# Optimization experiments

Measured on AMD Instinct MI355X. Metric: run time of the kernel, lower is better.

Reference implementation:

```python
import jax, jax.numpy as jnp
import numpy as np

N_NODES = 50000
N_EDGES = 800000
D_IN = 128
D_HID = 128
D_OUT = 128
N_GRAPHS = 512


def _linear_params(key, d_in, d_out):
    kw, kb = jax.random.split(key)
    bound = 1.0 / np.sqrt(d_in)
    W = jax.random.uniform(kw, (d_in, d_out), minval=-bound, maxval=bound, dtype=jnp.float32)
    b = jax.random.uniform(kb, (d_out,), minval=-bound, maxval=bound, dtype=jnp.float32)
    return W, b


def setup_inputs() -> dict:
    key = jax.random.key(0)
    ks = jax.random.split(key, 8)
    x = jax.random.normal(ks[0], (N_NODES, D_IN), dtype=jnp.float32)
    edge_index = jax.random.randint(ks[1], (2, N_EDGES), 0, N_NODES, dtype=jnp.int64)
    batch = jnp.sort(jax.random.randint(ks[2], (N_NODES,), 0, N_GRAPHS, dtype=jnp.int64))
    W1a, b1a = _linear_params(ks[3], D_IN, D_HID)
    W1b, b1b = _linear_params(ks[4], D_HID, D_HID)
    W2a, b2a = _linear_params(ks[5], D_HID, D_HID)
    W2b, b2b = _linear_params(ks[6], D_HID, D_OUT)
    Wfc, bfc = _linear_params(ks[7], D_OUT, D_OUT)
    return {"x": x, "edge_index": edge_index, "batch": batch,
            "W1a": W1a, "b1a": b1a, "W1b": W1b, "b1b": b1b,
            "W2a": W2a, "b2a": b2a, "W2b": W2b, "b2b": b2b,
            "Wfc": Wfc, "bfc": bfc}


def _gin_conv(h, src, dst, Wa, ba, Wb, bb):
    # neighbor sum: gather source features, scatter-add to targets (eps=0)
    agg = jax.ops.segment_sum(h[src], dst, num_segments=N_NODES)
    z = h + agg  # (1+eps)*x + sum_neighbors, eps=0
    z = jax.nn.relu(z @ Wa + ba)
    return z @ Wb + bb


def reference(x, edge_index, batch, W1a, b1a, W1b, b1b, W2a, b2a, W2b, b2b, Wfc, bfc):
    src, dst = edge_index[0], edge_index[1]
    h = jax.nn.relu(_gin_conv(x, src, dst, W1a, b1a, W1b, b1b))
    h = jax.nn.relu(_gin_conv(h, src, dst, W2a, b2a, W2b, b2b))
    g = jax.ops.segment_sum(h, batch, num_segments=N_GRAPHS)  # global_add_pool
    return jax.nn.relu(g @ Wfc + bfc)
```

## Files before the change

### kernel.cpp

```cpp
#include <hip/hip_runtime.h>

#define N_NODES 50000
#define N_EDGES 800000
#define N_GRAPHS 512
#define ZN N_NODES
#define BCAP 1536
#define RCAP 64
#define NBKT 782
#define EPB  8192
#define SCB  ((N_EDGES + EPB - 1) / EPB)

typedef __bf16 bf16x8 __attribute__((ext_vector_type(8)));
typedef float f32x4 __attribute__((ext_vector_type(4)));
typedef unsigned short u16;
typedef unsigned int u32;

__device__ __forceinline__ u16 f2bf(float f) {
    union { float f; u32 i; } v; v.f = f;
    u32 r = v.i + 0x7fffu + ((v.i >> 16) & 1u);
    return (u16)(r >> 16);
}
__device__ __forceinline__ float bf2f(u16 u) {
    union { u32 i; float f; } v; v.i = ((u32)u) << 16; return v.f;
}

__global__ __launch_bounds__(1024)
void k_prep(const int* __restrict__ ei, int* __restrict__ cur, u32* __restrict__ bins,
            const float* __restrict__ X, u16* __restrict__ XB, u16* __restrict__ HB,
            const float* __restrict__ W1a, const float* __restrict__ W1b,
            const float* __restrict__ W2a, const float* __restrict__ W2b,
            u16* __restrict__ T1a, u16* __restrict__ T1b,
            u16* __restrict__ T2a, u16* __restrict__ T2b,
            int E, int n8) {
    __shared__ int lcnt[NBKT];
    __shared__ int lpos[NBKT];
    int bid = blockIdx.x;
    int t = threadIdx.x;
    if (bid < SCB) {
        for (int i = t; i < NBKT; i += 1024) lcnt[i] = 0;
        __syncthreads();
        int e0 = bid * EPB;
        int sarr[8], barr[8], dlar[8];
#pragma unroll
        for (int k = 0; k < 8; ++k) {
            int e = e0 + k * 1024 + t;
            if (e < E) {
                int s = ei[e];
                int d = ei[E + e];
                sarr[k] = s; barr[k] = d >> 6; dlar[k] = d & 63;
                atomicAdd(&lcnt[d >> 6], 1);
            } else {
                barr[k] = -1; sarr[k] = 0; dlar[k] = 0;
            }
        }
        __syncthreads();
        for (int i = t; i < NBKT; i += 1024) {
            int c = lcnt[i];
            lpos[i] = (c > 0) ? atomicAdd(&cur[i * 32], c) : 0;
        }
        __syncthreads();
#pragma unroll
        for (int k = 0; k < 8; ++k) {
            if (barr[k] >= 0) {
                int p = atomicAdd(&lpos[barr[k]], 1);
                if (p < BCAP)
                    bins[(size_t)barr[k] * BCAP + p] = (((u32)dlar[k]) << 16) | (u32)sarr[k];
            }
        }
    } else if (bid < SCB + 782) {
        int i = (bid - SCB) * 1024 + t;
        if (i < n8) {
            float4 v0 = ((const float4*)X)[i * 2];
            float4 v1 = ((const float4*)X)[i * 2 + 1];
            uint4 o;
            o.x = (u32)f2bf(v0.x) | (((u32)f2bf(v0.y)) << 16);
            o.y = (u32)f2bf(v0.z) | (((u32)f2bf(v0.w)) << 16);
            o.z = (u32)f2bf(v1.x) | (((u32)f2bf(v1.y)) << 16);
            o.w = (u32)f2bf(v1.z) | (((u32)f2bf(v1.w)) << 16);
            ((uint4*)XB)[i] = o;
        }
    } else if (bid < SCB + 782 + 64) {
        int b2 = bid - (SCB + 782);
        int widx = b2 >> 4;
        int i = (b2 & 15) * 1024 + t;
        const float* W = widx == 0 ? W1a : widx == 1 ? W1b : widx == 2 ? W2a : W2b;
        u16* T = widx == 0 ? T1a : widx == 1 ? T1b : widx == 2 ? T2a : T2b;
        int k = i >> 7, n = i & 127;
        T[n * 128 + k] = f2bf(W[k * 128 + n]);
    } else {
        if (t < 64)       ((u32*)XB)[(size_t)ZN * 64 + t]        = 0u;
        else if (t < 128) ((u32*)HB)[(size_t)ZN * 64 + (t - 64)] = 0u;
    }
}


#define STAGE16(BUF, CI, CJ)                                            \
    _Pragma("unroll")                                                   \
    for (int u = 0; u < 16; ++u) {                                      \
        u32 nb = (u32)smI[wv * 8 + (CI)][(CJ) + u];                     \
        BUF[u] = X2[(nb << 6) + lane];                                  \
    }

#define ACCUM16(BUF)                                                    \
    _Pragma("unroll")                                                   \
    for (int u = 0; u < 16; ++u) {                                      \
        ax += bf2f((u16)(BUF[u] & 0xffff));                             \
        ay += bf2f((u16)(BUF[u] >> 16));                                \
    }

#define FINROW(CI) {                                                    \
        int r = wv * 8 + (CI);                                          \
        smZu[(r * 16 + ((lane >> 2) ^ (r & 15))) * 4 + (lane & 3)] =    \
            (((u32)f2bf(ay)) << 16) | (u32)f2bf(ax);                    \
        ax = 0.f; ay = 0.f;                                             \
    }

#define AGG_PHASE()                                                                  \
    {                                                                                \
        const u32 fill = 0xC350C350u;                      \
        int r = tid >> 3, c = tid & 7;                                               \
        uint4 v4 = make_uint4(fill, fill, fill, fill);                               \
        if (c == 0) {                                                                \
            int gr = row0 + r;                                                       \
            v4.x = (fill & 0xffff0000u) | (u32)((gr < N) ? gr : ZN);                 \
        }                                                                            \
        ((uint4*)smI)[tid] = v4;                                                     \
        if (tid < 64) ldsCnt[tid] = 1;                                               \
    }                                                                                \
    __syncthreads();                                                                 \
    {                                                                                \
        int ecnt = cur[blockIdx.x * 32];                                             \
        if (ecnt > BCAP) ecnt = BCAP;                                                \
        const u32* myb = bins + (size_t)blockIdx.x * BCAP;                           \
        for (int i = tid; i < ecnt; i += 512) {                                      \
            u32 v = myb[i];                                                          \
            int dl = v >> 16;                                                        \
            int pos = atomicAdd(&ldsCnt[dl], 1);                                     \
            if (pos < RCAP) smI[dl][pos] = (u16)(v & 0xffff);                        \
        }                                                                            \
    }                                                                                \
    __syncthreads();                                                                 \
    int degv = 0;                                                                    \
    if (lane < 8) {                                                                  \
        int d = ldsCnt[wv * 8 + lane];                                               \
        degv = d > RCAP ? RCAP : d;                                                  \
    }                                                                                \
    {                                                                                \
        float ax = 0.f, ay = 0.f;                                                    \
        u32 bufA[16], bufB[16];                                                      \
        int ci = 0, cj = 0;                                                          \
        int de = __builtin_amdgcn_readlane(degv, 0);                                 \
        STAGE16(bufA, 0, 0);                                                         \
        for (;;) {                                                                   \
            int ni = ci, nj = cj + 16;                                               \
            if (nj >= de) { ni = ci + 1; nj = 0; }                                   \
            int have = (ni < 8);                                                     \
            if (have) { de = __builtin_amdgcn_readlane(degv, ni);                    \
                        STAGE16(bufB, ni, nj); }                                     \
            ACCUM16(bufA);                                                           \
            if (nj == 0) FINROW(ci);                                                 \
            if (!have) break;                                                        \
            ci = ni; cj = nj;                                                        \
            ni = ci; nj = cj + 16;                                                   \
            if (nj >= de) { ni = ci + 1; nj = 0; }                                   \
            have = (ni < 8);                                                         \
            if (have) { de = __builtin_amdgcn_readlane(degv, ni);                    \
                        STAGE16(bufA, ni, nj); }                                     \
            ACCUM16(bufB);                                                           \
            if (nj == 0) FINROW(ci);                                                 \
            if (!have) break;                                                        \
            ci = ni; cj = nj;                                                        \
        }                                                                            \
    }

__global__ __launch_bounds__(512, 4)
void k_gin1(const u16* __restrict__ X, const int* __restrict__ cur,
            const u32* __restrict__ bins,
            const u16* __restrict__ WaT, const float* __restrict__ ba,
            const u16* __restrict__ WbT, const float* __restrict__ bb,
            u16* __restrict__ H, int N) {
    __shared__ u16 smZ[64 * 128];
    __shared__ u16 smW[128 * 128];
    __shared__ u16 smI[64][RCAP];
    __shared__ int ldsCnt[64];
    uint4* smZ4 = (uint4*)smZ;
    uint4* smW4 = (uint4*)smW;
    u32* smZu = (u32*)smZ;

    const int tid = threadIdx.x;
    const int lane = tid & 63, wv = tid >> 6;
    const int q = lane >> 4, m = lane & 15;
    const int ws = wv & 3, wc = wv >> 2;
    const int row0 = blockIdx.x * 64;
    const u32* X2 = (const u32*)X;

    for (int i = tid; i < 2048; i += 512) {
        int r = i >> 4, c4 = i & 15;
        smW4[r * 16 + (c4 ^ (r & 15))] = ((const uint4*)WaT)[i];
    }

    AGG_PHASE();
    __syncthreads();

    f32x4 acc[4];
#pragma unroll
    for (int nt = 0; nt < 4; ++nt) acc[nt] = (f32x4){0.f, 0.f, 0.f, 0.f};
#pragma unroll
    for (int kt = 0; kt < 4; ++kt) {
        int r = ws * 16 + m;
        bf16x8 a = *(const bf16x8*)(smZ4 + (r * 16 + ((kt * 4 + q) ^ (r & 15))));
#pragma unroll
        for (int nt = 0; nt < 4; ++nt) {
            int n = (wc * 4 + nt) * 16 + m;
            bf16x8 bfr = *(const bf16x8*)(smW4 + (n * 16 + ((kt * 4 + q) ^ (n & 15))));
            acc[nt] = __builtin_amdgcn_mfma_f32_16x16x32_bf16(a, bfr, acc[nt], 0, 0, 0);
        }
    }
    __syncthreads();

    for (int i = tid; i < 2048; i += 512) {
        int r = i >> 4, c4 = i & 15;
        smW4[r * 16 + (c4 ^ (r & 15))] = ((const uint4*)WbT)[i];
    }
#pragma unroll
    for (int nt = 0; nt < 4; ++nt) {
        int col = (wc * 4 + nt) * 16 + m;
        float bias = ba[col];
        int c4 = col >> 3, ci8 = col & 7;
#pragma unroll
        for (int r2 = 0; r2 < 4; ++r2) {
            int row = ws * 16 + q * 4 + r2;
            float x = acc[nt][r2] + bias;
            x = x > 0.f ? x : 0.f;
            smZ[(row * 16 + (c4 ^ (row & 15))) * 8 + ci8] = f2bf(x);
        }
    }
    __syncthreads();

    f32x4 acc2[4];
#pragma unroll
    for (int nt = 0; nt < 4; ++nt) acc2[nt] = (f32x4){0.f, 0.f, 0.f, 0.f};
#pragma unroll
    for (int kt = 0; kt < 4; ++kt) {
        int r = ws * 16 + m;
        bf16x8 a = *(const bf16x8*)(smZ4 + (r * 16 + ((kt * 4 + q) ^ (r & 15))));
#pragma unroll
        for (int nt = 0; nt < 4; ++nt) {
            int n = (wc * 4 + nt) * 16 + m;
            bf16x8 bfr = *(const bf16x8*)(smW4 + (n * 16 + ((kt * 4 + q) ^ (n & 15))));
            acc2[nt] = __builtin_amdgcn_mfma_f32_16x16x32_bf16(a, bfr, acc2[nt], 0, 0, 0);
        }
    }
#pragma unroll
    for (int nt = 0; nt < 4; ++nt) {
        int col = (wc * 4 + nt) * 16 + m;
        float bias = bb[col];
#pragma unroll
        for (int r2 = 0; r2 < 4; ++r2) {
            int row = row0 + ws * 16 + q * 4 + r2;
            if (row < N) {
                float x = acc2[nt][r2] + bias;
                H[(size_t)row * 128 + col] = f2bf(x > 0.f ? x : 0.f);
            }
        }
    }
}

__global__ __launch_bounds__(512, 4)
void k_gin2(const u16* __restrict__ X, const int* __restrict__ cur,
            const u32* __restrict__ bins,
            const u16* __restrict__ WaT, const float* __restrict__ ba,
            const u16* __restrict__ WbT, const float* __restrict__ bb,
            const int* __restrict__ batch, float* __restrict__ G, int N) {
    __shared__ u16 smZ[64 * 128];
    __shared__ u16 smW[128 * 128];
    __shared__ u16 smI[64][RCAP];
    __shared__ int ldsCnt[64];
    __shared__ int sb[64];
    uint4* smZ4 = (uint4*)smZ;
    uint4* smW4 = (uint4*)smW;
    u32* smZu = (u32*)smZ;

    const int tid = threadIdx.x;
    const int lane = tid & 63, wv = tid >> 6;
    const int q = lane >> 4, m = lane & 15;
    const int ws = wv & 3, wc = wv >> 2;
    const int row0 = blockIdx.x * 64;
    const u32* X2 = (const u32*)X;

    if (tid >= 448 && tid < 512) {
        int t = tid - 448;
        sb[t] = (row0 + t < N) ? batch[row0 + t] : -1;
    }

    for (int i = tid; i < 2048; i += 512) {
        int r = i >> 4, c4 = i & 15;
        smW4[r * 16 + (c4 ^ (r & 15))] = ((const uint4*)WaT)[i];
    }

    AGG_PHASE();
    __syncthreads();

    f32x4 acc[4];
#pragma unroll
    for (int nt = 0; nt < 4; ++nt) acc[nt] = (f32x4){0.f, 0.f, 0.f, 0.f};
#pragma unroll
    for (int kt = 0; kt < 4; ++kt) {
        int r = ws * 16 + m;
        bf16x8 a = *(const bf16x8*)(smZ4 + (r * 16 + ((kt * 4 + q) ^ (r & 15))));
#pragma unroll
        for (int nt = 0; nt < 4; ++nt) {
            int n = (wc * 4 + nt) * 16 + m;
            bf16x8 bfr = *(const bf16x8*)(smW4 + (n * 16 + ((kt * 4 + q) ^ (n & 15))));
            acc[nt] = __builtin_amdgcn_mfma_f32_16x16x32_bf16(a, bfr, acc[nt], 0, 0, 0);
        }
    }
    __syncthreads();

    for (int i = tid; i < 2048; i += 512) {
        int r = i >> 4, c4 = i & 15;
        smW4[r * 16 + (c4 ^ (r & 15))] = ((const uint4*)WbT)[i];
    }
#pragma unroll
    for (int nt = 0; nt < 4; ++nt) {
        int col = (wc * 4 + nt) * 16 + m;
        float bias = ba[col];
        int c4 = col >> 3, ci8 = col & 7;
#pragma unroll
        for (int r2 = 0; r2 < 4; ++r2) {
            int row = ws * 16 + q * 4 + r2;
            float x = acc[nt][r2] + bias;
            x = x > 0.f ? x : 0.f;
            smZ[(row * 16 + (c4 ^ (row & 15))) * 8 + ci8] = f2bf(x);
        }
    }
    __syncthreads();

    f32x4 acc2[4];
#pragma unroll
    for (int nt = 0; nt < 4; ++nt) acc2[nt] = (f32x4){0.f, 0.f, 0.f, 0.f};
#pragma unroll
    for (int kt = 0; kt < 4; ++kt) {
        int r = ws * 16 + m;
        bf16x8 a = *(const bf16x8*)(smZ4 + (r * 16 + ((kt * 4 + q) ^ (r & 15))));
#pragma unroll
        for (int nt = 0; nt < 4; ++nt) {
            int n = (wc * 4 + nt) * 16 + m;
            bf16x8 bfr = *(const bf16x8*)(smW4 + (n * 16 + ((kt * 4 + q) ^ (n & 15))));
            acc2[nt] = __builtin_amdgcn_mfma_f32_16x16x32_bf16(a, bfr, acc2[nt], 0, 0, 0);
        }
    }
#pragma unroll
    for (int nt = 0; nt < 4; ++nt) {
        int col = (wc * 4 + nt) * 16 + m;
        float bias = bb[col];
#pragma unroll
        for (int r2 = 0; r2 < 4; ++r2) {
            int row = ws * 16 + q * 4 + r2;
            float x = acc2[nt][r2] + bias;
            smZ[row * 128 + col] = f2bf(x > 0.f ? x : 0.f);
        }
    }
    __syncthreads();
    {
        int col = tid & 127, quarter = tid >> 7;
        int rbeg = quarter * 16, rend = rbeg + 16;
        float run = 0.f; int curg = -1;
        for (int r = rbeg; r < rend; ++r) {
            int gg = sb[r];
            if (gg < 0) break;
            if (gg != curg) {
                if (curg >= 0) atomicAdd(&G[curg * 128 + col], run);
                run = 0.f; curg = gg;
            }
            run += bf2f(smZ[r * 128 + col]);
        }
        if (curg >= 0) atomicAdd(&G[curg * 128 + col], run);
    }
}

__global__ void k_fc(const float* __restrict__ G, const float* __restrict__ W,
                     const float* __restrict__ bias, float* __restrict__ O) {
    __shared__ float gs[128];
    int t = threadIdx.x, gidx = blockIdx.x;
    gs[t] = G[gidx * 128 + t];
    __syncthreads();
    float acc = bias[t];
    for (int k = 0; k < 128; ++k)
        acc += gs[k] * W[k * 128 + t];
    acc = acc > 0.f ? acc : 0.f;
    O[gidx * 128 + t] = acc;
}

extern "C" void kernel_launch(void* const* d_in, const int* in_sizes, int n_in,
                              void* d_out, int out_size, void* d_ws, size_t ws_size,
                              hipStream_t stream) {
    const int N = N_NODES, E = N_EDGES, NG = N_GRAPHS;

    const float* x   = (const float*)d_in[0];
    const int* ei    = (const int*)d_in[1];
    const int* batch = (const int*)d_in[2];
    const float* W1a = (const float*)d_in[3];
    const float* b1a = (const float*)d_in[4];
    const float* W1b = (const float*)d_in[5];
    const float* b1b = (const float*)d_in[6];
    const float* W2a = (const float*)d_in[7];
    const float* b2a = (const float*)d_in[8];
    const float* W2b = (const float*)d_in[9];
    const float* b2b = (const float*)d_in[10];
    const float* Wfc = (const float*)d_in[11];
    const float* bfc = (const float*)d_in[12];
    float* out = (float*)d_out;

    char* w = (char*)d_ws;
    int* cur    = (int*)(w + 0x0000000);
    float* g    = (float*)(w + 0x0019000);
    u32* bins   = (u32*)(w + 0x0060000);
    u16* xb     = (u16*)(w + 0x0500000);
    u16* hb     = (u16*)(w + 0x1200000);
    u16* T1a    = (u16*)(w + 0x1F00000);
    u16* T1b    = (u16*)(w + 0x1F08000);
    u16* T2a    = (u16*)(w + 0x1F10000);
    u16* T2b    = (u16*)(w + 0x1F18000);

    (void)hipMemsetAsync(w, 0, 0x59000, stream);

    const int n8 = N * 128 / 8;
    const int PREPB = SCB + 782 + 64 + 1;
    k_prep<<<PREPB, 1024, 0, stream>>>(ei, cur, bins, x, xb, hb, W1a, W1b, W2a, W2b,
                                       T1a, T1b, T2a, T2b, E, n8);

    const int GINB = (N + 63) / 64;

    k_gin1<<<GINB, 512, 0, stream>>>(xb, cur, bins, T1a, b1a, T1b, b1b, hb, N);
    k_gin2<<<GINB, 512, 0, stream>>>(hb, cur, bins, T2a, b2a, T2b, b2b, batch, g, N);

    k_fc<<<NG, 128, 0, stream>>>(g, Wfc, bfc, out);
}
```

Before: 196.8 us.

## Replace global-atomic edge binning with histogram, prefix-scan, and deterministic placement

Edge bucketing is split into three kernels: per-block bucket histograms, a per-bucket prefix scan across blocks, and a placement pass that writes each edge at its computed offset. This removes the global atomicAdd on the per-bucket cursors and makes bin order deterministic, which may improve locality in the later gathers. The cost is two extra kernel launches, a second read of the edge indices, and extra workspace for the hist and base arrays.

```diff
diff --git a/kernel.cpp b/kernel.cpp
--- a/kernel.cpp
+++ b/kernel.cpp
@@ -25,48 +25,27 @@
 }
 
 __global__ __launch_bounds__(1024)
-void k_prep(const int* __restrict__ ei, int* __restrict__ cur, u32* __restrict__ bins,
-            const float* __restrict__ X, u16* __restrict__ XB, u16* __restrict__ HB,
-            const float* __restrict__ W1a, const float* __restrict__ W1b,
-            const float* __restrict__ W2a, const float* __restrict__ W2b,
-            u16* __restrict__ T1a, u16* __restrict__ T1b,
-            u16* __restrict__ T2a, u16* __restrict__ T2b,
-            int E, int n8) {
+void k_prepA(const int* __restrict__ ei, int* __restrict__ hist,
+             const float* __restrict__ X, u16* __restrict__ XB, u16* __restrict__ HB,
+             const float* __restrict__ W1a, const float* __restrict__ W1b,
+             const float* __restrict__ W2a, const float* __restrict__ W2b,
+             u16* __restrict__ T1a, u16* __restrict__ T1b,
+             u16* __restrict__ T2a, u16* __restrict__ T2b,
+             int E, int n8) {
     __shared__ int lcnt[NBKT];
-    __shared__ int lpos[NBKT];
     int bid = blockIdx.x;
     int t = threadIdx.x;
     if (bid < SCB) {
         for (int i = t; i < NBKT; i += 1024) lcnt[i] = 0;
         __syncthreads();
         int e0 = bid * EPB;
-        int sarr[8], barr[8], dlar[8];
 #pragma unroll
         for (int k = 0; k < 8; ++k) {
             int e = e0 + k * 1024 + t;
-            if (e < E) {
-                int s = ei[e];
-                int d = ei[E + e];
-                sarr[k] = s; barr[k] = d >> 6; dlar[k] = d & 63;
-                atomicAdd(&lcnt[d >> 6], 1);
-            } else {
-                barr[k] = -1; sarr[k] = 0; dlar[k] = 0;
-            }
+            if (e < E) atomicAdd(&lcnt[ei[E + e] >> 6], 1);
         }
         __syncthreads();
-        for (int i = t; i < NBKT; i += 1024) {
-            int c = lcnt[i];
-            lpos[i] = (c > 0) ? atomicAdd(&cur[i * 32], c) : 0;
-        }
-        __syncthreads();
-#pragma unroll
-        for (int k = 0; k < 8; ++k) {
-            if (barr[k] >= 0) {
-                int p = atomicAdd(&lpos[barr[k]], 1);
-                if (p < BCAP)
-                    bins[(size_t)barr[k] * BCAP + p] = (((u32)dlar[k]) << 16) | (u32)sarr[k];
-            }
-        }
+        for (int i = t; i < NBKT; i += 1024) hist[bid * NBKT + i] = lcnt[i];
     } else if (bid < SCB + 782) {
         int i = (bid - SCB) * 1024 + t;
         if (i < n8) {
@@ -90,6 +69,63 @@
     } else {
         if (t < 64)       ((u32*)XB)[(size_t)ZN * 64 + t]        = 0u;
         else if (t < 128) ((u32*)HB)[(size_t)ZN * 64 + (t - 64)] = 0u;
+    }
+}
+
+__global__ __launch_bounds__(512)
+void k_prefix(const int* __restrict__ hist, int* __restrict__ base, int* __restrict__ cur) {
+    int j = blockIdx.x * 8 + (threadIdx.x >> 6);
+    int lane = threadIdx.x & 63;
+    if (j >= NBKT) return;
+    int v0 = hist[lane * NBKT + j];
+    int v1 = (lane < SCB - 64) ? hist[(64 + lane) * NBKT + j] : 0;
+    int x0 = v0, x1 = v1;
+#pragma unroll
+    for (int off = 1; off < 64; off <<= 1) {
+        int t0 = __shfl_up(x0, off);
+        int t1 = __shfl_up(x1, off);
+        if (lane >= off) { x0 += t0; x1 += t1; }
+    }
+    int sum0 = __shfl(x0, 63);
+    base[lane * NBKT + j] = x0 - v0;
+    if (lane < SCB - 64) base[(64 + lane) * NBKT + j] = sum0 + x1 - v1;
+    int tot = sum0 + __shfl(x1, 63);
+    if (lane == 0) cur[j * 32] = tot;
+}
+
+__global__ __launch_bounds__(1024)
+void k_place(const int* __restrict__ ei, const int* __restrict__ base,
+             u32* __restrict__ bins, int E) {
+    __shared__ int lcnt[NBKT];
+    __shared__ int lbase[NBKT];
+    int bid = blockIdx.x;
+    int t = threadIdx.x;
+    for (int i = t; i < NBKT; i += 1024) {
+        lcnt[i] = 0;
+        lbase[i] = base[bid * NBKT + i];
+    }
+    __syncthreads();
+    int e0 = bid * EPB;
+    int sarr[8], barr[8], dlar[8], rank[8];
+#pragma unroll
+    for (int k = 0; k < 8; ++k) {
+        int e = e0 + k * 1024 + t;
+        if (e < E) {
+            int s = ei[e];
+            int d = ei[E + e];
+            sarr[k] = s; barr[k] = d >> 6; dlar[k] = d & 63;
+            rank[k] = atomicAdd(&lcnt[d >> 6], 1);
+        } else {
+            barr[k] = -1; sarr[k] = 0; dlar[k] = 0; rank[k] = 0;
+        }
+    }
+#pragma unroll
+    for (int k = 0; k < 8; ++k) {
+        if (barr[k] >= 0) {
+            int pos = lbase[barr[k]] + rank[k];
+            if (pos < BCAP)
+                bins[(size_t)barr[k] * BCAP + pos] = (((u32)dlar[k]) << 16) | (u32)sarr[k];
+        }
     }
 }
 
@@ -415,20 +451,24 @@
     char* w = (char*)d_ws;
     int* cur    = (int*)(w + 0x0000000);
     float* g    = (float*)(w + 0x0019000);
-    u32* bins   = (u32*)(w + 0x0060000);
-    u16* xb     = (u16*)(w + 0x0500000);
-    u16* hb     = (u16*)(w + 0x1200000);
-    u16* T1a    = (u16*)(w + 0x1F00000);
-    u16* T1b    = (u16*)(w + 0x1F08000);
-    u16* T2a    = (u16*)(w + 0x1F10000);
-    u16* T2b    = (u16*)(w + 0x1F18000);
+    int* hist   = (int*)(w + 0x0059000);
+    int* base   = (int*)(w + 0x00A5000);
+    u32* bins   = (u32*)(w + 0x0100000);
+    u16* xb     = (u16*)(w + 0x0600000);
+    u16* hb     = (u16*)(w + 0x1400000);
+    u16* T1a    = (u16*)(w + 0x2200000);
+    u16* T1b    = (u16*)(w + 0x2208000);
+    u16* T2a    = (u16*)(w + 0x2210000);
+    u16* T2b    = (u16*)(w + 0x2218000);
 
     (void)hipMemsetAsync(w, 0, 0x59000, stream);
 
     const int n8 = N * 128 / 8;
     const int PREPB = SCB + 782 + 64 + 1;
-    k_prep<<<PREPB, 1024, 0, stream>>>(ei, cur, bins, x, xb, hb, W1a, W1b, W2a, W2b,
-                                       T1a, T1b, T2a, T2b, E, n8);
+    k_prepA<<<PREPB, 1024, 0, stream>>>(ei, hist, x, xb, hb, W1a, W1b, W2a, W2b,
+                                        T1a, T1b, T2a, T2b, E, n8);
+    k_prefix<<<(NBKT + 7) / 8, 512, 0, stream>>>(hist, base, cur);
+    k_place<<<SCB, 1024, 0, stream>>>(ei, base, bins, E);
 
     const int GINB = (N + 63) / 64;
 
```

New measurement: 203.0 us. 1.03x slower.
